# Optimization experiments

Measured on AMD Instinct MI355X. Metric: run time of the kernel, lower is better.

## Reference

```python
import jax, jax.numpy as jnp
import numpy as np
import math

H = 12   # num_attention_heads
DH = 64  # attention_head_size
HID = H * DH  # 768


def setup_inputs() -> dict:
    key = jax.random.key(0)
    ks = jax.random.split(key, 16)
    B, S = 2, 128
    inp = {
        'hidden_states': jax.random.normal(ks[0], (B, S, HID), jnp.float32),
        'attention_mask': jnp.zeros((B, 1, 1, S), jnp.float32),
        'inference_path': jax.random.normal(ks[1], (B, S, S, HID), jnp.float32),
        'span_mask': jax.random.uniform(ks[2], (B, 1, S, S), jnp.float32),
    }
    sc = 1.0 / math.sqrt(HID)
    # weights stored as [in, out]; y = x @ W + b
    inp['Wq'] = jax.random.normal(ks[3], (HID, HID), jnp.float32) * sc
    inp['bq'] = jnp.zeros((HID,), jnp.float32)
    inp['Wk'] = jax.random.normal(ks[4], (HID, HID), jnp.float32) * sc
    inp['bk'] = jnp.zeros((HID,), jnp.float32)
    inp['Wv'] = jax.random.normal(ks[5], (HID, HID), jnp.float32) * sc
    inp['bv'] = jnp.zeros((HID,), jnp.float32)
    inp['Wpv'] = jax.random.normal(ks[6], (HID, DH), jnp.float32) * sc
    inp['bpv'] = jnp.zeros((DH,), jnp.float32)
    inp['Wip'] = jax.random.normal(ks[7], (HID, 2 * HID), jnp.float32) * sc
    inp['Wmlp'] = jax.random.normal(ks[8], (HID + DH, HID), jnp.float32) * sc
    inp['bmlp'] = jnp.zeros((HID,), jnp.float32)
    return inp


def reference(hidden_states, attention_mask, inference_path, span_mask,
              Wq, bq, Wk, bk, Wv, bv, Wpv, bpv, Wip, Wmlp, bmlp):
    B, S, _ = hidden_states.shape
    # projections
    q = (hidden_states @ Wq + bq).reshape(B, S, H, DH).transpose(0, 2, 1, 3)  # [B,H,S,Dh]
    k = (hidden_states @ Wk + bk).reshape(B, S, H, DH).transpose(0, 2, 1, 3)
    v = (hidden_states @ Wv + bv).reshape(B, S, H, DH).transpose(0, 2, 1, 3)
    # parse value path: [B,1,S,Dh]
    pv = (hidden_states @ Wpv + bpv).reshape(B, S, 1, DH).transpose(0, 2, 1, 3)
    parse_ctx = jnp.matmul(span_mask, pv)              # [B,1,S,Dh]
    parse_ctx = parse_ctx.transpose(0, 2, 1, 3)        # [B,S,1,Dh]
    # relative inference-path bias: raw view (matches torch .view semantics)
    ip = inference_path @ Wip                           # [B,S,S,2*HID]
    ra, rb = jnp.split(ip, 2, axis=-1)                  # each [B,S,S,HID]
    ra = ra.reshape(B, H, S, S, DH)
    rb = rb.reshape(B, H, S, S, DH)
    qe = q[:, :, :, None, :] + ra                       # [B,H,S,S,Dh]
    ke = k[:, :, None, :, :] + rb                       # [B,H,S,S,Dh]
    scores = jnp.einsum('bhqkd,bhqkd->bhqk', qe, ke)
    scores = scores / math.sqrt(DH) + attention_mask
    probs = jax.nn.softmax(scores, axis=-1)             # dropout is identity in eval
    ctx = jnp.matmul(probs, v)                          # [B,H,S,Dh]
    ctx = ctx.transpose(0, 2, 1, 3)                     # [B,S,H,Dh]
    ctx = jnp.concatenate([ctx, parse_ctx], axis=-2)    # [B,S,H+1,Dh]
    ctx = ctx.reshape(B, S, HID + DH)
    return ctx @ Wmlp + bmlp                            # [B,S,HID]
```

## Files before the change

### kernel.cpp

```cpp
#include <hip/hip_runtime.h>
#include <hip/hip_bf16.h>


typedef __attribute__((ext_vector_type(8))) __bf16 bf16x8;
typedef __attribute__((ext_vector_type(16))) float f32x16;
typedef __attribute__((ext_vector_type(4))) float f32x4;

#define QKV_OFF   0u
#define ARENA_OFF 2424832u
#define SC_OFF    4784128u
#define CTX_OFF   6356992u

__global__ __launch_bounds__(256)
void prep_kernel(const float* __restrict__ Wip, __bf16* __restrict__ arena) {
  const int l = threadIdx.x & 63;
  const int f = blockIdx.x * 4 + (threadIdx.x >> 6);
  const int n32 = f / 48, k16 = f - n32 * 48;
  const float* src = Wip + (size_t)(k16 * 16 + (l >> 5) * 8) * 1536 + n32 * 32 + (l & 31);
  union { __bf16 h[8]; uint4 u; } pk;
#pragma unroll
  for (int j = 0; j < 8; j++) pk.h[j] = (__bf16)src[(size_t)j * 1536];
  ((uint4*)arena)[(size_t)f * 64 + l] = pk.u;
}

__global__ __launch_bounds__(64)
void proj_kernel(const float* __restrict__ hs,
                 const float* __restrict__ Wq, const float* __restrict__ bq,
                 const float* __restrict__ Wk, const float* __restrict__ bk,
                 const float* __restrict__ Wv, const float* __restrict__ bv,
                 const float* __restrict__ Wpv, const float* __restrict__ bpv,
                 float* __restrict__ qkv) {
  const int n0 = blockIdx.x * 32;
  const int m0 = blockIdx.y * 32;
  const float* W; const float* bias; int noff, ldw;
  if (n0 < 768)       { W = Wq;  bias = bq;  noff = n0;        ldw = 768; }
  else if (n0 < 1536) { W = Wk;  bias = bk;  noff = n0 - 768;  ldw = 768; }
  else if (n0 < 2304) { W = Wv;  bias = bv;  noff = n0 - 1536; ldw = 768; }
  else                { W = Wpv; bias = bpv; noff = n0 - 2304; ldw = 64;  }
  const int l = threadIdx.x;
  const int rsel = l & 31, ksel = l >> 5;
  f32x16 acc;
#pragma unroll
  for (int z = 0; z < 16; z++) acc[z] = 0.f;

#pragma unroll 4
  for (int k16 = 0; k16 < 48; k16++) {
    const float* ap = hs + (size_t)(m0 + rsel) * 768 + k16 * 16 + ksel * 8;
    float4 a0 = *(const float4*)ap;
    float4 a1 = *(const float4*)(ap + 4);
    union { __bf16 h[8]; bf16x8 v; } pa;
    pa.h[0] = (__bf16)a0.x; pa.h[1] = (__bf16)a0.y; pa.h[2] = (__bf16)a0.z; pa.h[3] = (__bf16)a0.w;
    pa.h[4] = (__bf16)a1.x; pa.h[5] = (__bf16)a1.y; pa.h[6] = (__bf16)a1.z; pa.h[7] = (__bf16)a1.w;
    const float* bp = W + (size_t)(k16 * 16 + ksel * 8) * ldw + noff + rsel;
    union { __bf16 h[8]; bf16x8 v; } pb;
#pragma unroll
    for (int j = 0; j < 8; j++) pb.h[j] = (__bf16)bp[(size_t)j * ldw];
    acc = __builtin_amdgcn_mfma_f32_32x32x16_bf16(pa.v, pb.v, acc, 0, 0, 0);
  }
#pragma unroll
  for (int reg = 0; reg < 16; reg++) {
    int row = (reg & 3) + ((reg >> 2) << 3) + (ksel << 2);
    qkv[(size_t)(m0 + row) * 2368 + n0 + rsel] = acc[reg] + bias[noff + rsel];
  }
}

extern __shared__ char smem_raw[];

__global__ __launch_bounds__(512, 2)
void score_kernel(const float* __restrict__ infp,
                  const __bf16* __restrict__ arena,
                  const float* __restrict__ qkv,
                  float* __restrict__ scores) {
  char* Abase = smem_raw;
  float* lds_sc = (float*)(smem_raw + 99840);
  const int tid = threadIdx.x;
  const int lane = tid & 63;
  const int ml = lane & 31;
  const int kh = lane >> 5;
  const int wv = tid >> 6;
  const int wc = wv & 3;
  const int wd = wv >> 2;
  const int blk = blockIdx.x;
  const int b = blk >> 8;
  const int r0 = (blk & 255) << 6;

  for (int z = tid; z < 768; z += 512) lds_sc[z] = 0.f;

  const uint4* BA = (const uint4*)arena;
  const uint4* bptr  = BA + (size_t)((2 * wc + wd) * 48) * 64 + lane;
  const uint4* bptr2 = bptr + 73728;
  int kpn = 0;
  uint4 B0[8], B1[8], B2[8];
  bf16x8 Af[8];
  f32x16 acc_ra[2], acc_rb[2];

  auto loadB = [&](uint4* dst) {
#pragma unroll
    for (int ks = 0; ks < 4; ks++) {
      dst[ks * 2]     = bptr[ks * 64];
      dst[ks * 2 + 1] = bptr2[ks * 64];
    }
    if (kpn == 11) { bptr += 21760; bptr2 += 21760; kpn = 0; }
    else           { bptr += 256;   bptr2 += 256;   kpn++;  }
  };

  loadB(B0);
  loadB(B1);

  {
    const f32x4* A4 = (const f32x4*)(infp + (size_t)(b * 16384 + r0) * 768);
#pragma unroll
    for (int p = 0; p < 12; p++) {
      int idx = p * 512 + tid;
      int m = (int)(((unsigned)idx * 10923u) >> 20);
      int g = idx - m * 96;
      f32x4 v0 = __builtin_nontemporal_load(A4 + m * 192 + g * 2);
      f32x4 v1 = __builtin_nontemporal_load(A4 + m * 192 + g * 2 + 1);
      union { __bf16 h[8]; uint4 u; } pk;
      pk.h[0] = (__bf16)v0[0]; pk.h[1] = (__bf16)v0[1];
      pk.h[2] = (__bf16)v0[2]; pk.h[3] = (__bf16)v0[3];
      pk.h[4] = (__bf16)v1[0]; pk.h[5] = (__bf16)v1[1];
      pk.h[6] = (__bf16)v1[2]; pk.h[7] = (__bf16)v1[3];
      int F = (m >> 5) * 48 + (g >> 1);
      int slot = (m & 31) + ((g & 1) << 5);
      *(uint4*)(Abase + ((F * 65 + slot) << 4)) = pk.u;
    }
  }
  __syncthreads();

  const size_t lane_off = (size_t)(lane << 4);
  auto loadA = [&](int kcc) {
    const char* ab = Abase + lane_off + kcc * 4160;
#pragma unroll
    for (int mt = 0; mt < 2; mt++)
#pragma unroll
      for (int ks = 0; ks < 4; ks++)
        Af[mt * 4 + ks] = *(const bf16x8*)(ab + mt * 49920 + ks * 1040);
  };
  auto mfma_step = [&](const uint4* Bb) {
#pragma unroll
    for (int ks = 0; ks < 4; ks++) {
      bf16x8 bra = *(const bf16x8*)&Bb[ks * 2];
      bf16x8 brb = *(const bf16x8*)&Bb[ks * 2 + 1];
#pragma unroll
      for (int mt = 0; mt < 2; mt++) {
        acc_ra[mt] = __builtin_amdgcn_mfma_f32_32x32x16_bf16(Af[mt * 4 + ks], bra, acc_ra[mt], 0, 0, 0);
        acc_rb[mt] = __builtin_amdgcn_mfma_f32_32x32x16_bf16(Af[mt * 4 + ks], brb, acc_rb[mt], 0, 0, 0);
      }
    }
  };
  auto epilogue = [&](int c) {
    int d = wd * 32 + ml;
#pragma unroll
    for (int mt = 0; mt < 2; mt++) {
      float qv[16], kv[16];
#pragma unroll
      for (int reg = 0; reg < 16; reg++) {
        int row = mt * 32 + (reg & 3) + ((reg >> 2) << 3) + (kh << 2);
        int t = 12 * (r0 + row) + c;
        int hh = t >> 14;
        int ii = (t >> 7) & 127;
        int jj = t & 127;
        qv[reg] = qkv[(size_t)((b << 7) + ii) * 2368 + (hh << 6) + d];
        kv[reg] = qkv[(size_t)((b << 7) + jj) * 2368 + 768 + (hh << 6) + d];
      }
#pragma unroll
      for (int reg = 0; reg < 16; reg++) {
        int row = mt * 32 + (reg & 3) + ((reg >> 2) << 3) + (kh << 2);
        float p = (qv[reg] + acc_ra[mt][reg]) * (kv[reg] + acc_rb[mt][reg]);
        p += __shfl_xor(p, 16);
        p += __shfl_xor(p, 8);
        p += __shfl_xor(p, 4);
        p += __shfl_xor(p, 2);
        p += __shfl_xor(p, 1);
        if (ml == 0) atomicAdd(&lds_sc[row * 12 + c], p);
      }
    }
#pragma unroll
    for (int mt = 0; mt < 2; mt++)
#pragma unroll
      for (int z = 0; z < 16; z++) { acc_ra[mt][z] = 0.f; acc_rb[mt][z] = 0.f; }
  };

#pragma unroll
  for (int mt = 0; mt < 2; mt++)
#pragma unroll
    for (int z = 0; z < 16; z++) { acc_ra[mt][z] = 0.f; acc_rb[mt][z] = 0.f; }

  int kcc = 0, cc = wc;
#pragma unroll 1
  for (int it = 0; it < 12; it++) {
    {
      loadB(B2);
      loadA(kcc);
      mfma_step(B0);
      if (kcc == 11) { epilogue(cc); kcc = 0; cc += 4; } else kcc++;
    }
    {
      if (it < 11) loadB(B0);
      loadA(kcc);
      mfma_step(B1);
      if (kcc == 11) { epilogue(cc); kcc = 0; cc += 4; } else kcc++;
    }
    {
      if (it < 11) loadB(B1);
      loadA(kcc);
      mfma_step(B2);
      if (kcc == 11) { epilogue(cc); kcc = 0; cc += 4; } else kcc++;
    }
  }

  __syncthreads();
  for (int z = tid; z < 768; z += 512) {
    int row = z / 12;
    int ccc = z - row * 12;
    int t = 12 * (r0 + row) + ccc;
    int hh = t >> 14;
    int ii = (t >> 7) & 127;
    int jj = t & 127;
    scores[(size_t)((b * 12 + hh) * 128 + ii) * 128 + jj] = lds_sc[z];
  }
}

__global__ __launch_bounds__(256)
void attn_kernel(const float* __restrict__ scores, const float* __restrict__ qkv,
                 const float* __restrict__ mask, const float* __restrict__ span,
                 float* __restrict__ ctx) {
  const int i = blockIdx.x;
  const int b = blockIdx.y;
  const int tid = threadIdx.x;
  const int l = tid & 63;
  const int wvi = tid >> 6;
  __shared__ float w[13][132];
  for (int r = wvi; r < 13; r += 4) {
    if (r < 12) {
      const float* sp = scores + (size_t)((b * 12 + r) * 128 + i) * 128;
      float s0 = sp[l] * 0.125f + mask[b * 128 + l];
      float s1 = sp[l + 64] * 0.125f + mask[b * 128 + l + 64];
      float mx = fmaxf(s0, s1);
#pragma unroll
      for (int o = 32; o; o >>= 1) mx = fmaxf(mx, __shfl_xor(mx, o));
      float e0 = __expf(s0 - mx), e1 = __expf(s1 - mx);
      float sm = e0 + e1;
#pragma unroll
      for (int o = 32; o; o >>= 1) sm += __shfl_xor(sm, o);
      float inv = 1.f / sm;
      w[r][l] = e0 * inv;
      w[r][l + 64] = e1 * inv;
    } else {
      const float* sp = span + (size_t)(b * 128 + i) * 128;
      w[12][l] = sp[l];
      w[12][l + 64] = sp[l + 64];
    }
  }
  __syncthreads();
  for (int o = tid; o < 832; o += 256) {
    int h = o >> 6, d = o & 63;
    const float* vp = qkv + (size_t)(b * 128) * 2368 + (h < 12 ? 1536 + h * 64 : 2304) + d;
    float acc = 0.f;
#pragma unroll 8
    for (int j = 0; j < 128; j++) acc += w[h][j] * vp[(size_t)j * 2368];
    ctx[(size_t)(b * 128 + i) * 832 + o] = acc;
  }
}

__global__ __launch_bounds__(64)
void out_kernel(const float* __restrict__ ctxb, const float* __restrict__ Wmlp,
                const float* __restrict__ bmlp, float* __restrict__ out) {
  const int n0 = blockIdx.x * 32;
  const int m0 = blockIdx.y * 32;
  const int l = threadIdx.x;
  const int rsel = l & 31, ksel = l >> 5;
  f32x16 acc;
#pragma unroll
  for (int z = 0; z < 16; z++) acc[z] = 0.f;

#pragma unroll 4
  for (int k16 = 0; k16 < 52; k16++) {
    const float* ap = ctxb + (size_t)(m0 + rsel) * 832 + k16 * 16 + ksel * 8;
    float4 a0 = *(const float4*)ap;
    float4 a1 = *(const float4*)(ap + 4);
    union { __bf16 h[8]; bf16x8 v; } pa;
    pa.h[0] = (__bf16)a0.x; pa.h[1] = (__bf16)a0.y; pa.h[2] = (__bf16)a0.z; pa.h[3] = (__bf16)a0.w;
    pa.h[4] = (__bf16)a1.x; pa.h[5] = (__bf16)a1.y; pa.h[6] = (__bf16)a1.z; pa.h[7] = (__bf16)a1.w;
    const float* bp = Wmlp + (size_t)(k16 * 16 + ksel * 8) * 768 + n0 + rsel;
    union { __bf16 h[8]; bf16x8 v; } pb;
#pragma unroll
    for (int j = 0; j < 8; j++) pb.h[j] = (__bf16)bp[(size_t)j * 768];
    acc = __builtin_amdgcn_mfma_f32_32x32x16_bf16(pa.v, pb.v, acc, 0, 0, 0);
  }
#pragma unroll
  for (int reg = 0; reg < 16; reg++) {
    int row = (reg & 3) + ((reg >> 2) << 3) + (ksel << 2);
    out[(size_t)(m0 + row) * 768 + n0 + rsel] = acc[reg] + bmlp[n0 + rsel];
  }
}

extern "C" void kernel_launch(void* const* d_in, const int* in_sizes, int n_in,
                              void* d_out, int out_size, void* d_ws, size_t ws_size,
                              hipStream_t stream) {
  const float* hs   = (const float*)d_in[0];
  const float* mask = (const float*)d_in[1];
  const float* infp = (const float*)d_in[2];
  const float* span = (const float*)d_in[3];
  const float* Wq   = (const float*)d_in[4];
  const float* bq   = (const float*)d_in[5];
  const float* Wk   = (const float*)d_in[6];
  const float* bk   = (const float*)d_in[7];
  const float* Wv   = (const float*)d_in[8];
  const float* bv   = (const float*)d_in[9];
  const float* Wpv  = (const float*)d_in[10];
  const float* bpv  = (const float*)d_in[11];
  const float* Wip  = (const float*)d_in[12];
  const float* Wmlp = (const float*)d_in[13];
  const float* bmlp = (const float*)d_in[14];
  float* out = (float*)d_out;

  char* ws = (char*)d_ws;
  float*  qkv    = (float*)(ws + QKV_OFF);
  __bf16* arena  = (__bf16*)(ws + ARENA_OFF);
  float*  scores = (float*)(ws + SC_OFF);
  float*  ctx    = (float*)(ws + CTX_OFF);

  prep_kernel<<<dim3(576), 256, 0, stream>>>(Wip, arena);
  proj_kernel<<<dim3(74, 8), 64, 0, stream>>>(hs, Wq, bq, Wk, bk, Wv, bv, Wpv, bpv, qkv);
  score_kernel<<<dim3(512), 512, 102912, stream>>>(infp, arena, qkv, scores);
  attn_kernel<<<dim3(128, 2), 256, 0, stream>>>(scores, qkv, mask, span, ctx);
  out_kernel<<<dim3(24, 8), 64, 0, stream>>>(ctx, Wmlp, bmlp, out);
}
```

Baseline: 354.3 us.

## Split ra/rb accumulation across two wave groups with LDS handoff in score kernel

Doubles the score kernel block to 1024 threads. One group of 8 waves computes the ra projection and the other the rb projection, each holding one accumulator set instead of two, with ra results handed to the rb waves through LDS for the epilogue dot product. It also drops the LDS row padding (stride 65 to 64) and moves from triple to double buffering of B fragments. The aim is lower register pressure and more waves in flight. The cost is two extra block-wide barriers per epilogue, possible LDS bank conflicts from the removed padding, and larger dynamic LDS, which likely limits occupancy to one block per CU.

```diff
diff --git a/kernel.cpp b/kernel.cpp
--- a/kernel.cpp
+++ b/kernel.cpp
@@ -66,52 +66,49 @@
 
 extern __shared__ char smem_raw[];
 
-__global__ __launch_bounds__(512, 2)
+__global__ __launch_bounds__(1024, 4)
 void score_kernel(const float* __restrict__ infp,
                   const __bf16* __restrict__ arena,
                   const float* __restrict__ qkv,
                   float* __restrict__ scores) {
   char* Abase = smem_raw;
-  float* lds_sc = (float*)(smem_raw + 99840);
+  float* lds_sc = (float*)(smem_raw + 98304);
+  float* hand   = (float*)(smem_raw + 101376);
   const int tid = threadIdx.x;
   const int lane = tid & 63;
   const int ml = lane & 31;
   const int kh = lane >> 5;
   const int wv = tid >> 6;
-  const int wc = wv & 3;
-  const int wd = wv >> 2;
+  const int wv8 = wv & 7;
+  const int wr = wv >> 3;
+  const int wc = wv8 & 3;
+  const int wd = wv8 >> 2;
   const int blk = blockIdx.x;
   const int b = blk >> 8;
   const int r0 = (blk & 255) << 6;
 
-  for (int z = tid; z < 768; z += 512) lds_sc[z] = 0.f;
-
-  const uint4* BA = (const uint4*)arena;
-  const uint4* bptr  = BA + (size_t)((2 * wc + wd) * 48) * 64 + lane;
-  const uint4* bptr2 = bptr + 73728;
+  for (int z = tid; z < 768; z += 1024) lds_sc[z] = 0.f;
+
+  const uint4* bptr = (const uint4*)arena + (size_t)((2 * wc + wd) * 48) * 64
+                      + (size_t)wr * 73728 + lane;
   int kpn = 0;
-  uint4 B0[8], B1[8], B2[8];
+  bf16x8 B0[4], B1[4];
   bf16x8 Af[8];
-  f32x16 acc_ra[2], acc_rb[2];
-
-  auto loadB = [&](uint4* dst) {
-#pragma unroll
-    for (int ks = 0; ks < 4; ks++) {
-      dst[ks * 2]     = bptr[ks * 64];
-      dst[ks * 2 + 1] = bptr2[ks * 64];
-    }
-    if (kpn == 11) { bptr += 21760; bptr2 += 21760; kpn = 0; }
-    else           { bptr += 256;   bptr2 += 256;   kpn++;  }
+  f32x16 acc[2];
+
+  auto loadB = [&](bf16x8* dst) {
+#pragma unroll
+    for (int ks = 0; ks < 4; ks++) dst[ks] = *(const bf16x8*)(bptr + ks * 64);
+    if (kpn == 11) { bptr += 21760; kpn = 0; } else { bptr += 256; kpn++; }
   };
 
   loadB(B0);
-  loadB(B1);
 
   {
     const f32x4* A4 = (const f32x4*)(infp + (size_t)(b * 16384 + r0) * 768);
 #pragma unroll
-    for (int p = 0; p < 12; p++) {
-      int idx = p * 512 + tid;
+    for (int p = 0; p < 6; p++) {
+      int idx = p * 1024 + tid;
       int m = (int)(((unsigned)idx * 10923u) >> 20);
       int g = idx - m * 96;
       f32x4 v0 = __builtin_nontemporal_load(A4 + m * 192 + g * 2);
@@ -123,95 +120,101 @@
       pk.h[6] = (__bf16)v1[2]; pk.h[7] = (__bf16)v1[3];
       int F = (m >> 5) * 48 + (g >> 1);
       int slot = (m & 31) + ((g & 1) << 5);
-      *(uint4*)(Abase + ((F * 65 + slot) << 4)) = pk.u;
+      *(uint4*)(Abase + ((F * 64 + slot) << 4)) = pk.u;
     }
   }
   __syncthreads();
 
-  const size_t lane_off = (size_t)(lane << 4);
+  const int lane_off = lane << 4;
   auto loadA = [&](int kcc) {
-    const char* ab = Abase + lane_off + kcc * 4160;
+    const char* ab = Abase + lane_off + kcc * 4096;
 #pragma unroll
     for (int mt = 0; mt < 2; mt++)
 #pragma unroll
       for (int ks = 0; ks < 4; ks++)
-        Af[mt * 4 + ks] = *(const bf16x8*)(ab + mt * 49920 + ks * 1040);
+        Af[mt * 4 + ks] = *(const bf16x8*)(ab + mt * 49152 + ks * 1024);
   };
-  auto mfma_step = [&](const uint4* Bb) {
-#pragma unroll
-    for (int ks = 0; ks < 4; ks++) {
-      bf16x8 bra = *(const bf16x8*)&Bb[ks * 2];
-      bf16x8 brb = *(const bf16x8*)&Bb[ks * 2 + 1];
-#pragma unroll
-      for (int mt = 0; mt < 2; mt++) {
-        acc_ra[mt] = __builtin_amdgcn_mfma_f32_32x32x16_bf16(Af[mt * 4 + ks], bra, acc_ra[mt], 0, 0, 0);
-        acc_rb[mt] = __builtin_amdgcn_mfma_f32_32x32x16_bf16(Af[mt * 4 + ks], brb, acc_rb[mt], 0, 0, 0);
-      }
-    }
+  auto mfma_step = [&](const bf16x8* Bb) {
+#pragma unroll
+    for (int ks = 0; ks < 4; ks++)
+#pragma unroll
+      for (int mt = 0; mt < 2; mt++)
+        acc[mt] = __builtin_amdgcn_mfma_f32_32x32x16_bf16(Af[mt * 4 + ks], Bb[ks], acc[mt], 0, 0, 0);
   };
   auto epilogue = [&](int c) {
-    int d = wd * 32 + ml;
+    const int d = wd * 32 + ml;
 #pragma unroll
     for (int mt = 0; mt < 2; mt++) {
-      float qv[16], kv[16];
-#pragma unroll
-      for (int reg = 0; reg < 16; reg++) {
-        int row = mt * 32 + (reg & 3) + ((reg >> 2) << 3) + (kh << 2);
-        int t = 12 * (r0 + row) + c;
-        int hh = t >> 14;
-        int ii = (t >> 7) & 127;
-        int jj = t & 127;
-        qv[reg] = qkv[(size_t)((b << 7) + ii) * 2368 + (hh << 6) + d];
-        kv[reg] = qkv[(size_t)((b << 7) + jj) * 2368 + 768 + (hh << 6) + d];
+      if (wr == 0) {
+#pragma unroll
+        for (int q = 0; q < 4; q++) {
+          f32x4 w4;
+          w4[0] = acc[mt][q * 4 + 0]; w4[1] = acc[mt][q * 4 + 1];
+          w4[2] = acc[mt][q * 4 + 2]; w4[3] = acc[mt][q * 4 + 3];
+          *(f32x4*)(hand + (wv8 * 4 + q) * 256 + lane * 4) = w4;
+        }
       }
-#pragma unroll
-      for (int reg = 0; reg < 16; reg++) {
-        int row = mt * 32 + (reg & 3) + ((reg >> 2) << 3) + (kh << 2);
-        float p = (qv[reg] + acc_ra[mt][reg]) * (kv[reg] + acc_rb[mt][reg]);
-        p += __shfl_xor(p, 16);
-        p += __shfl_xor(p, 8);
-        p += __shfl_xor(p, 4);
-        p += __shfl_xor(p, 2);
-        p += __shfl_xor(p, 1);
-        if (ml == 0) atomicAdd(&lds_sc[row * 12 + c], p);
+      __syncthreads();
+      if (wr == 1) {
+#pragma unroll
+        for (int q = 0; q < 4; q++) {
+          f32x4 ra4 = *(const f32x4*)(hand + (wv8 * 4 + q) * 256 + lane * 4);
+          float qv[4], kv[4];
+#pragma unroll
+          for (int j = 0; j < 4; j++) {
+            int row = mt * 32 + j + q * 8 + (kh << 2);
+            int t = 12 * (r0 + row) + c;
+            int hh = t >> 14;
+            int ii = (t >> 7) & 127;
+            int jj = t & 127;
+            qv[j] = qkv[(size_t)((b << 7) + ii) * 2368 + (hh << 6) + d];
+            kv[j] = qkv[(size_t)((b << 7) + jj) * 2368 + 768 + (hh << 6) + d];
+          }
+#pragma unroll
+          for (int j = 0; j < 4; j++) {
+            int row = mt * 32 + j + q * 8 + (kh << 2);
+            float p = (qv[j] + ra4[j]) * (kv[j] + acc[mt][q * 4 + j]);
+            p += __shfl_xor(p, 16);
+            p += __shfl_xor(p, 8);
+            p += __shfl_xor(p, 4);
+            p += __shfl_xor(p, 2);
+            p += __shfl_xor(p, 1);
+            if (ml == 0) atomicAdd(&lds_sc[row * 12 + c], p);
+          }
+        }
       }
+      __syncthreads();
     }
 #pragma unroll
     for (int mt = 0; mt < 2; mt++)
 #pragma unroll
-      for (int z = 0; z < 16; z++) { acc_ra[mt][z] = 0.f; acc_rb[mt][z] = 0.f; }
+      for (int z = 0; z < 16; z++) acc[mt][z] = 0.f;
   };
 
 #pragma unroll
   for (int mt = 0; mt < 2; mt++)
 #pragma unroll
-    for (int z = 0; z < 16; z++) { acc_ra[mt][z] = 0.f; acc_rb[mt][z] = 0.f; }
-
-  int kcc = 0, cc = wc;
+    for (int z = 0; z < 16; z++) acc[mt][z] = 0.f;
+
+  int kc = 0, c = wc;
 #pragma unroll 1
-  for (int it = 0; it < 12; it++) {
+  for (int it = 0; it < 18; it++) {
     {
-      loadB(B2);
-      loadA(kcc);
+      loadB(B1);
+      loadA(kc);
       mfma_step(B0);
-      if (kcc == 11) { epilogue(cc); kcc = 0; cc += 4; } else kcc++;
+      if (kc == 11) { epilogue(c); kc = 0; c += 4; } else kc++;
     }
     {
-      if (it < 11) loadB(B0);
-      loadA(kcc);
+      if (it < 17) loadB(B0);
+      loadA(kc);
       mfma_step(B1);
-      if (kcc == 11) { epilogue(cc); kcc = 0; cc += 4; } else kcc++;
-    }
-    {
-      if (it < 11) loadB(B1);
-      loadA(kcc);
-      mfma_step(B2);
-      if (kcc == 11) { epilogue(cc); kcc = 0; cc += 4; } else kcc++;
+      if (kc == 11) { epilogue(c); kc = 0; c += 4; } else kc++;
     }
   }
 
   __syncthreads();
-  for (int z = tid; z < 768; z += 512) {
+  for (int z = tid; z < 768; z += 1024) {
     int row = z / 12;
     int ccc = z - row * 12;
     int t = 12 * (r0 + row) + ccc;
@@ -324,7 +327,7 @@
 
   prep_kernel<<<dim3(576), 256, 0, stream>>>(Wip, arena);
   proj_kernel<<<dim3(74, 8), 64, 0, stream>>>(hs, Wq, bq, Wk, bk, Wv, bv, Wpv, bpv, qkv);
-  score_kernel<<<dim3(512), 512, 102912, stream>>>(infp, arena, qkv, scores);
+  score_kernel<<<dim3(512), 1024, 134144, stream>>>(infp, arena, qkv, scores);
   attn_kernel<<<dim3(128, 2), 256, 0, stream>>>(scores, qkv, mask, span, ctx);
   out_kernel<<<dim3(24, 8), 64, 0, stream>>>(ctx, Wmlp, bmlp, out);
 }
```

Result: slower. 368.0 us (+3.9%).

## Use raw buffer loads with explicit vmcnt waits for triple-buffered B prefetch

Applied to the files above, without the earlier changes.

Replaces the compiler-generated global loads of the bf16 Wip fragments with inline-asm buffer_load_dwordx4 through a buffer resource descriptor. Three register banks are now kept in flight, and explicit s_waitcnt vmcnt counts with sched barriers control when each bank is consumed. The last iteration is peeled. The goal is to keep B prefetches outstanding across MFMA steps so the compiler cannot insert conservative full waits. The risk is that manual vmcnt accounting can go wrong if the compiler issues other vector-memory ops in between, and the sched barriers restrict instruction scheduling.

```diff
diff --git a/kernel.cpp b/kernel.cpp
--- a/kernel.cpp
+++ b/kernel.cpp
@@ -5,6 +5,7 @@
 typedef __attribute__((ext_vector_type(8))) __bf16 bf16x8;
 typedef __attribute__((ext_vector_type(16))) float f32x16;
 typedef __attribute__((ext_vector_type(4))) float f32x4;
+typedef __attribute__((ext_vector_type(4))) unsigned int u32x4;
 
 #define QKV_OFF   0u
 #define ARENA_OFF 2424832u
@@ -86,26 +87,42 @@
 
   for (int z = tid; z < 768; z += 512) lds_sc[z] = 0.f;
 
-  const uint4* BA = (const uint4*)arena;
-  const uint4* bptr  = BA + (size_t)((2 * wc + wd) * 48) * 64 + lane;
-  const uint4* bptr2 = bptr + 73728;
+  u32x4 srsrc;
+  srsrc[0] = (unsigned)(unsigned long long)arena;
+  srsrc[1] = (unsigned)(((unsigned long long)arena) >> 32);
+  srsrc[2] = 2359296u;
+  srsrc[3] = 0x00020000u;
+  const unsigned rbo = 1179648u;
+  unsigned voff = (unsigned)((2 * wc + wd) * 49152 + lane * 16);
   int kpn = 0;
-  uint4 B0[8], B1[8], B2[8];
+
+  u32x4 B0[8], B1[8], B2[8];
   bf16x8 Af[8];
   f32x16 acc_ra[2], acc_rb[2];
 
-  auto loadB = [&](uint4* dst) {
-#pragma unroll
-    for (int ks = 0; ks < 4; ks++) {
-      dst[ks * 2]     = bptr[ks * 64];
-      dst[ks * 2 + 1] = bptr2[ks * 64];
-    }
-    if (kpn == 11) { bptr += 21760; bptr2 += 21760; kpn = 0; }
-    else           { bptr += 256;   bptr2 += 256;   kpn++;  }
+  auto issueB = [&](u32x4* bank) {
+    asm volatile("buffer_load_dwordx4 %0, %1, %2, 0 offen offset:0"
+                 : "=&v"(bank[0]) : "v"(voff), "s"(srsrc));
+    asm volatile("buffer_load_dwordx4 %0, %1, %2, 0 offen offset:1024"
+                 : "=&v"(bank[2]) : "v"(voff), "s"(srsrc));
+    asm volatile("buffer_load_dwordx4 %0, %1, %2, 0 offen offset:2048"
+                 : "=&v"(bank[4]) : "v"(voff), "s"(srsrc));
+    asm volatile("buffer_load_dwordx4 %0, %1, %2, 0 offen offset:3072"
+                 : "=&v"(bank[6]) : "v"(voff), "s"(srsrc));
+    asm volatile("buffer_load_dwordx4 %0, %1, %2, %3 offen offset:0"
+                 : "=&v"(bank[1]) : "v"(voff), "s"(srsrc), "s"(rbo));
+    asm volatile("buffer_load_dwordx4 %0, %1, %2, %3 offen offset:1024"
+                 : "=&v"(bank[3]) : "v"(voff), "s"(srsrc), "s"(rbo));
+    asm volatile("buffer_load_dwordx4 %0, %1, %2, %3 offen offset:2048"
+                 : "=&v"(bank[5]) : "v"(voff), "s"(srsrc), "s"(rbo));
+    asm volatile("buffer_load_dwordx4 %0, %1, %2, %3 offen offset:3072"
+                 : "=&v"(bank[7]) : "v"(voff), "s"(srsrc), "s"(rbo));
+    if (kpn == 11) { voff += 348160u; kpn = 0; } else { voff += 4096u; kpn++; }
   };
 
-  loadB(B0);
-  loadB(B1);
+  issueB(B0);
+  issueB(B1);
+  issueB(B2);
 
   {
     const f32x4* A4 = (const f32x4*)(infp + (size_t)(b * 16384 + r0) * 768);
@@ -137,11 +154,11 @@
       for (int ks = 0; ks < 4; ks++)
         Af[mt * 4 + ks] = *(const bf16x8*)(ab + mt * 49920 + ks * 1040);
   };
-  auto mfma_step = [&](const uint4* Bb) {
+  auto mfma_step = [&](const u32x4* Bb) {
 #pragma unroll
     for (int ks = 0; ks < 4; ks++) {
-      bf16x8 bra = *(const bf16x8*)&Bb[ks * 2];
-      bf16x8 brb = *(const bf16x8*)&Bb[ks * 2 + 1];
+      bf16x8 bra = __builtin_bit_cast(bf16x8, Bb[ks * 2]);
+      bf16x8 brb = __builtin_bit_cast(bf16x8, Bb[ks * 2 + 1]);
 #pragma unroll
       for (int mt = 0; mt < 2; mt++) {
         acc_ra[mt] = __builtin_amdgcn_mfma_f32_32x32x16_bf16(Af[mt * 4 + ks], bra, acc_ra[mt], 0, 0, 0);
@@ -187,28 +204,33 @@
 #pragma unroll
     for (int z = 0; z < 16; z++) { acc_ra[mt][z] = 0.f; acc_rb[mt][z] = 0.f; }
 
-  int kcc = 0, cc = wc;
+#define WAIT16 do { asm volatile("s_waitcnt vmcnt(16)" ::: "memory"); __builtin_amdgcn_sched_barrier(0); } while (0)
+#define WAIT8  do { asm volatile("s_waitcnt vmcnt(8)"  ::: "memory"); __builtin_amdgcn_sched_barrier(0); } while (0)
+#define WAIT0  do { asm volatile("s_waitcnt vmcnt(0)"  ::: "memory"); __builtin_amdgcn_sched_barrier(0); } while (0)
+
+  int kc = 0, c = wc;
 #pragma unroll 1
-  for (int it = 0; it < 12; it++) {
+  for (int it = 0; it < 11; it++) {
     {
-      loadB(B2);
-      loadA(kcc);
-      mfma_step(B0);
-      if (kcc == 11) { epilogue(cc); kcc = 0; cc += 4; } else kcc++;
+      loadA(kc); WAIT16; mfma_step(B0); issueB(B0);
+      if (kc == 11) { epilogue(c); kc = 0; c += 4; } else kc++;
     }
     {
-      if (it < 11) loadB(B0);
-      loadA(kcc);
-      mfma_step(B1);
-      if (kcc == 11) { epilogue(cc); kcc = 0; cc += 4; } else kcc++;
+      loadA(kc); WAIT16; mfma_step(B1); issueB(B1);
+      if (kc == 11) { epilogue(c); kc = 0; c += 4; } else kc++;
     }
     {
-      if (it < 11) loadB(B1);
-      loadA(kcc);
-      mfma_step(B2);
-      if (kcc == 11) { epilogue(cc); kcc = 0; cc += 4; } else kcc++;
-    }
-  }
+      loadA(kc); WAIT16; mfma_step(B2); issueB(B2);
+      if (kc == 11) { epilogue(c); kc = 0; c += 4; } else kc++;
+    }
+  }
+  loadA(kc); WAIT16; mfma_step(B0); kc++;
+  loadA(kc); WAIT8;  mfma_step(B1); kc++;
+  loadA(kc); WAIT0;  mfma_step(B2); epilogue(c);
+
+#undef WAIT16
+#undef WAIT8
+#undef WAIT0
 
   __syncthreads();
   for (int z = tid; z < 768; z += 512) {
```

Result: slower. 408.8 us (+15.4%).

## Split score kernel across column halves with XCD-aware mapping and merge prep/proj

Applied to the files above, without the earlier changes.

The score kernel now uses 768-thread blocks and twice as many blocks. Each block handles one half of the 12 column groups (6 per block, one per wave pair) instead of looping over all 12, and the block index is remapped so the two halves of a row tile land on different XCD groups. Each wave now runs a single 12-step K loop with one epilogue, removing the pointer-wrap bookkeeping. The cost is that the infp tile is loaded and converted to bf16 twice, once by each half-block. The Wip prep and QKV projection kernels are fused into one launch with 4 waves per projection block, removing a launch and improving occupancy for the projection.

```diff
diff --git a/kernel.cpp b/kernel.cpp
--- a/kernel.cpp
+++ b/kernel.cpp
@@ -12,32 +12,33 @@
 #define CTX_OFF   6356992u
 
 __global__ __launch_bounds__(256)
-void prep_kernel(const float* __restrict__ Wip, __bf16* __restrict__ arena) {
-  const int l = threadIdx.x & 63;
-  const int f = blockIdx.x * 4 + (threadIdx.x >> 6);
-  const int n32 = f / 48, k16 = f - n32 * 48;
-  const float* src = Wip + (size_t)(k16 * 16 + (l >> 5) * 8) * 1536 + n32 * 32 + (l & 31);
-  union { __bf16 h[8]; uint4 u; } pk;
-#pragma unroll
-  for (int j = 0; j < 8; j++) pk.h[j] = (__bf16)src[(size_t)j * 1536];
-  ((uint4*)arena)[(size_t)f * 64 + l] = pk.u;
-}
-
-__global__ __launch_bounds__(64)
-void proj_kernel(const float* __restrict__ hs,
-                 const float* __restrict__ Wq, const float* __restrict__ bq,
-                 const float* __restrict__ Wk, const float* __restrict__ bk,
-                 const float* __restrict__ Wv, const float* __restrict__ bv,
-                 const float* __restrict__ Wpv, const float* __restrict__ bpv,
-                 float* __restrict__ qkv) {
-  const int n0 = blockIdx.x * 32;
-  const int m0 = blockIdx.y * 32;
+void prep_proj_kernel(const float* __restrict__ Wip, __bf16* __restrict__ arena,
+                      const float* __restrict__ hs,
+                      const float* __restrict__ Wq, const float* __restrict__ bq,
+                      const float* __restrict__ Wk, const float* __restrict__ bk,
+                      const float* __restrict__ Wv, const float* __restrict__ bv,
+                      const float* __restrict__ Wpv, const float* __restrict__ bpv,
+                      float* __restrict__ qkv) {
+  if (blockIdx.x < 576) {
+    const int l = threadIdx.x & 63;
+    const int f = blockIdx.x * 4 + (threadIdx.x >> 6);
+    const int n32 = f / 48, k16 = f - n32 * 48;
+    const float* src = Wip + (size_t)(k16 * 16 + (l >> 5) * 8) * 1536 + n32 * 32 + (l & 31);
+    union { __bf16 h[8]; uint4 u; } pk;
+#pragma unroll
+    for (int j = 0; j < 8; j++) pk.h[j] = (__bf16)src[(size_t)j * 1536];
+    ((uint4*)arena)[(size_t)f * 64 + l] = pk.u;
+    return;
+  }
+  const int pblk = blockIdx.x - 576;
+  const int n0 = (pblk % 74) * 32;
+  const int m0 = (pblk / 74) * 128 + (threadIdx.x >> 6) * 32;
   const float* W; const float* bias; int noff, ldw;
   if (n0 < 768)       { W = Wq;  bias = bq;  noff = n0;        ldw = 768; }
   else if (n0 < 1536) { W = Wk;  bias = bk;  noff = n0 - 768;  ldw = 768; }
   else if (n0 < 2304) { W = Wv;  bias = bv;  noff = n0 - 1536; ldw = 768; }
   else                { W = Wpv; bias = bpv; noff = n0 - 2304; ldw = 64;  }
-  const int l = threadIdx.x;
+  const int l = threadIdx.x & 63;
   const int rsel = l & 31, ksel = l >> 5;
   f32x16 acc;
 #pragma unroll
@@ -66,7 +67,7 @@
 
 extern __shared__ char smem_raw[];
 
-__global__ __launch_bounds__(512, 2)
+__global__ __launch_bounds__(768, 1)
 void score_kernel(const float* __restrict__ infp,
                   const __bf16* __restrict__ arena,
                   const float* __restrict__ qkv,
@@ -78,18 +79,21 @@
   const int ml = lane & 31;
   const int kh = lane >> 5;
   const int wv = tid >> 6;
-  const int wc = wv & 3;
-  const int wd = wv >> 2;
+  const int wd = (wv >= 6) ? 1 : 0;
+  const int cc = wv - 6 * wd;
   const int blk = blockIdx.x;
-  const int b = blk >> 8;
-  const int r0 = (blk & 255) << 6;
-
-  for (int z = tid; z < 768; z += 512) lds_sc[z] = 0.f;
-
-  const uint4* BA = (const uint4*)arena;
-  const uint4* bptr  = BA + (size_t)((2 * wc + wd) * 48) * 64 + lane;
+  const int xcd = blk & 7;
+  const int chalf = xcd >> 2;
+  const int id = ((blk >> 3) << 2) + (xcd & 3);
+  const int b = id >> 8;
+  const int r0 = (id & 255) << 6;
+  const int c = chalf * 6 + cc;
+  const int n32 = 2 * c + wd;
+
+  if (tid < 384) lds_sc[tid] = 0.f;
+
+  const uint4* bptr  = (const uint4*)arena + (size_t)(n32 * 48) * 64 + lane;
   const uint4* bptr2 = bptr + 73728;
-  int kpn = 0;
   uint4 B0[8], B1[8], B2[8];
   bf16x8 Af[8];
   f32x16 acc_ra[2], acc_rb[2];
@@ -100,8 +104,7 @@
       dst[ks * 2]     = bptr[ks * 64];
       dst[ks * 2 + 1] = bptr2[ks * 64];
     }
-    if (kpn == 11) { bptr += 21760; bptr2 += 21760; kpn = 0; }
-    else           { bptr += 256;   bptr2 += 256;   kpn++;  }
+    bptr += 256; bptr2 += 256;
   };
 
   loadB(B0);
@@ -110,8 +113,8 @@
   {
     const f32x4* A4 = (const f32x4*)(infp + (size_t)(b * 16384 + r0) * 768);
 #pragma unroll
-    for (int p = 0; p < 12; p++) {
-      int idx = p * 512 + tid;
+    for (int p = 0; p < 8; p++) {
+      int idx = p * 768 + tid;
       int m = (int)(((unsigned)idx * 10923u) >> 20);
       int g = idx - m * 96;
       f32x4 v0 = __builtin_nontemporal_load(A4 + m * 192 + g * 2);
@@ -140,8 +143,8 @@
   auto mfma_step = [&](const uint4* Bb) {
 #pragma unroll
     for (int ks = 0; ks < 4; ks++) {
-      bf16x8 bra = *(const bf16x8*)&Bb[ks * 2];
-      bf16x8 brb = *(const bf16x8*)&Bb[ks * 2 + 1];
+      bf16x8 bra = __builtin_bit_cast(bf16x8, Bb[ks * 2]);
+      bf16x8 brb = __builtin_bit_cast(bf16x8, Bb[ks * 2 + 1]);
 #pragma unroll
       for (int mt = 0; mt < 2; mt++) {
         acc_ra[mt] = __builtin_amdgcn_mfma_f32_32x32x16_bf16(Af[mt * 4 + ks], bra, acc_ra[mt], 0, 0, 0);
@@ -149,8 +152,31 @@
       }
     }
   };
-  auto epilogue = [&](int c) {
-    int d = wd * 32 + ml;
+
+#pragma unroll
+  for (int mt = 0; mt < 2; mt++)
+#pragma unroll
+    for (int z = 0; z < 16; z++) { acc_ra[mt][z] = 0.f; acc_rb[mt][z] = 0.f; }
+
+  int kcs = 0;
+#pragma unroll 1
+  for (int it = 0; it < 4; it++) {
+    {
+      loadB(B2);
+      loadA(kcs); mfma_step(B0); kcs++;
+    }
+    {
+      if (it < 3) loadB(B0);
+      loadA(kcs); mfma_step(B1); kcs++;
+    }
+    {
+      if (it < 3) loadB(B1);
+      loadA(kcs); mfma_step(B2); kcs++;
+    }
+  }
+
+  {
+    const int d = wd * 32 + ml;
 #pragma unroll
     for (int mt = 0; mt < 2; mt++) {
       float qv[16], kv[16];
@@ -173,52 +199,21 @@
         p += __shfl_xor(p, 4);
         p += __shfl_xor(p, 2);
         p += __shfl_xor(p, 1);
-        if (ml == 0) atomicAdd(&lds_sc[row * 12 + c], p);
+        if (ml == 0) atomicAdd(&lds_sc[row * 6 + cc], p);
       }
     }
-#pragma unroll
-    for (int mt = 0; mt < 2; mt++)
-#pragma unroll
-      for (int z = 0; z < 16; z++) { acc_ra[mt][z] = 0.f; acc_rb[mt][z] = 0.f; }
-  };
-
-#pragma unroll
-  for (int mt = 0; mt < 2; mt++)
-#pragma unroll
-    for (int z = 0; z < 16; z++) { acc_ra[mt][z] = 0.f; acc_rb[mt][z] = 0.f; }
-
-  int kcc = 0, cc = wc;
-#pragma unroll 1
-  for (int it = 0; it < 12; it++) {
-    {
-      loadB(B2);
-      loadA(kcc);
-      mfma_step(B0);
-      if (kcc == 11) { epilogue(cc); kcc = 0; cc += 4; } else kcc++;
-    }
-    {
-      if (it < 11) loadB(B0);
-      loadA(kcc);
-      mfma_step(B1);
-      if (kcc == 11) { epilogue(cc); kcc = 0; cc += 4; } else kcc++;
-    }
-    {
-      if (it < 11) loadB(B1);
-      loadA(kcc);
-      mfma_step(B2);
-      if (kcc == 11) { epilogue(cc); kcc = 0; cc += 4; } else kcc++;
-    }
   }
 
   __syncthreads();
-  for (int z = tid; z < 768; z += 512) {
-    int row = z / 12;
-    int ccc = z - row * 12;
-    int t = 12 * (r0 + row) + ccc;
+  if (tid < 384) {
+    int row = tid / 6;
+    int c2 = chalf * 6 + (tid - row * 6);
+    int t = 12 * (r0 + row) + c2;
     int hh = t >> 14;
     int ii = (t >> 7) & 127;
     int jj = t & 127;
-    scores[(size_t)((b * 12 + hh) * 128 + ii) * 128 + jj] = lds_sc[z];
+    __builtin_nontemporal_store(lds_sc[tid],
+        scores + (size_t)((b * 12 + hh) * 128 + ii) * 128 + jj);
   }
 }
 
@@ -322,9 +317,9 @@
   float*  scores = (float*)(ws + SC_OFF);
   float*  ctx    = (float*)(ws + CTX_OFF);
 
-  prep_kernel<<<dim3(576), 256, 0, stream>>>(Wip, arena);
-  proj_kernel<<<dim3(74, 8), 64, 0, stream>>>(hs, Wq, bq, Wk, bk, Wv, bv, Wpv, bpv, qkv);
-  score_kernel<<<dim3(512), 512, 102912, stream>>>(infp, arena, qkv, scores);
+  prep_proj_kernel<<<dim3(724), 256, 0, stream>>>(Wip, arena, hs,
+      Wq, bq, Wk, bk, Wv, bv, Wpv, bpv, qkv);
+  score_kernel<<<dim3(1024), 768, 101376, stream>>>(infp, arena, qkv, scores);
   attn_kernel<<<dim3(128, 2), 256, 0, stream>>>(scores, qkv, mask, span, ctx);
   out_kernel<<<dim3(24, 8), 64, 0, stream>>>(ctx, Wmlp, bmlp, out);
 }
```

Result: slower. 378.5 us (+6.8%).
